# Kernel tuning notes

Measured on AMD Instinct MI355X. Metric: run time of the kernel, lower is better.

The kernel has to match this reference:

```python
import jax, jax.numpy as jnp
import numpy as np

# iRPE contextual+transposed, method=PRODUCT, rpe config ratio=1.9
ALPHA, BETA, GAMMA = 1.9, 3.8, 15.2
BETA_INT = int(BETA)            # 3
S = 2 * BETA_INT + 1            # 7
NUM_BUCKETS = S * S             # 49
B, H, D = 8, 8, 64
HEIGHT = WIDTH = 32
L = HEIGHT * WIDTH              # 1024, skip = L - height*width = 0


def _piecewise_index(rp):
    # numpy port of torch piecewise_index (no-grad, precomputed constant)
    rp = np.asarray(rp)
    rp_abs = np.abs(rp)
    safe = np.maximum(rp_abs.astype(np.float64), ALPHA)  # avoid log(0) under mask
    y = ALPHA + np.log(safe / ALPHA) / np.log(GAMMA / ALPHA) * (BETA - ALPHA)
    y = np.minimum(np.round(y), BETA)                    # round then clip(max=beta)
    out = np.where(rp_abs <= ALPHA, np.round(rp.astype(np.float64)), np.sign(rp) * y)
    return out.astype(np.int64)                          # trunc toward zero (+-3.8 -> +-3)


def _rp_bucket_product(height, width):
    pos = np.stack(np.meshgrid(np.arange(height), np.arange(width), indexing='ij'), -1)
    pos = pos.reshape(-1, 2)                             # (L, 2)
    diff = pos[:, None, :] - pos[None, :, :]             # (L, L, 2)
    r = _piecewise_index(diff[:, :, 0]) + BETA_INT
    c = _piecewise_index(diff[:, :, 1]) + BETA_INT
    return (r * S + c).astype(np.int32)                  # values in [0, 49)


def setup_inputs() -> dict:
    key = jax.random.key(0)
    k1, k2 = jax.random.split(key)
    x = jax.random.normal(k1, (B, H, L, D), dtype=jnp.float32)
    lookup_table_weight = jax.random.normal(k2, (H, D, NUM_BUCKETS), dtype=jnp.float32) * 0.02
    rp_bucket = jnp.asarray(_rp_bucket_product(HEIGHT, WIDTH))  # (L, L) int32 constant
    return {"x": x, "lookup_table_weight": lookup_table_weight, "rp_bucket": rp_bucket}


def reference(x, lookup_table_weight, rp_bucket):
    # x: (B, H, L, D); lookup_table_weight: (H, D, K); rp_bucket: (L, L) int
    # lt[b,h,l,k] = sum_d x[b,h,l,d] * W[h,d,k]
    lt = jnp.einsum('bhld,hdk->bhlk', x, lookup_table_weight)  # (B, H, L, K) small
    Lq = rp_bucket.shape[0]
    row = jnp.arange(Lq)[:, None]                              # (L, 1)
    # out[b,h,i,j] = lt[b,h,i,rp_bucket[i,j]] -- the big irregular gather
    return lt[:, :, row, rp_bucket]                            # (B, H, L, L)
```

## Files before the change

### kernel.cpp

```cpp
#include <hip/hip_runtime.h>


constexpr int cL = 1024;
constexpr int cD = 64;
constexpr int cK = 49;
constexpr int cBH = 64;
constexpr int cHALF = 32;

__global__ __launch_bounds__(256) void irpe_fused(
    const float* __restrict__ x,
    const float* __restrict__ W,
    const int*   __restrict__ bucket,
    float*       __restrict__ out)
{
    __shared__ float4 xs4[cHALF][cD / 4];
    __shared__ float  lts[cHALF * cK];

    const int gid  = blockIdx.x;
    const int i    = gid >> 1;
    const int bh0  = (gid & 1) * cHALF;
    const int tid  = threadIdx.x;

    const float4* x4 = (const float4*)x;
    #pragma unroll
    for (int r = 0; r < 2; ++r) {
        const int idx = r * 256 + tid;
        const int lh  = idx >> 4;
        const int d4  = idx & 15;
        xs4[lh][d4] = x4[((size_t)(bh0 + lh) * cL + i) * (cD / 4) + d4];
    }

    const int4 bk = ((const int4*)(bucket + (size_t)i * cL))[tid];

    __syncthreads();

    const float* xsf = (const float*)xs4;
    for (int p = tid; p < cHALF * cK; p += 256) {
        const int lh = p / cK;
        const int k  = p - lh * cK;
        const int h  = (bh0 + lh) & 7;
        const float* wp = W + (size_t)h * cD * cK + k;
        const float* xr = xsf + lh * cD;
        float acc = 0.0f;
        #pragma unroll
        for (int d = 0; d < cD; ++d) {
            acc = fmaf(xr[d], wp[(size_t)d * cK], acc);
        }
        lts[p] = acc;
    }
    __syncthreads();

    float4* obase = (float4*)(out + (size_t)bh0 * cL * cL + (size_t)i * cL);
    #pragma unroll 4
    for (int lh = 0; lh < cHALF; ++lh) {
        const float* lrow = lts + lh * cK;
        float4 o;
        o.x = lrow[bk.x];
        o.y = lrow[bk.y];
        o.z = lrow[bk.z];
        o.w = lrow[bk.w];
        obase[(size_t)lh * cL * (cL / 4) + tid] = o;
    }
}

extern "C" void kernel_launch(void* const* d_in, const int* in_sizes, int n_in,
                              void* d_out, int out_size, void* d_ws, size_t ws_size,
                              hipStream_t stream) {
    const float* x      = (const float*)d_in[0];
    const float* W      = (const float*)d_in[1];
    const int*   bucket = (const int*)d_in[2];
    float*       out    = (float*)d_out;

    const int grid = cL * 2;
    irpe_fused<<<grid, 256, 0, stream>>>(x, W, bucket, out);
}
```

Baseline: 320.4 us.

## Retile iRPE gather over 4 query rows by 16 batch-heads per block

Each block now covers 4 consecutive query rows and 16 batch-head slices instead of 1 row and 32 slices. Each wavefront owns 4 batch-heads and writes 4 contiguous output rows (16 KB) per slice. The bucket rows are held in 16 int4 registers per lane and reused across batch-heads. This is meant to give longer contiguous write streams and to amortize bucket loads, at the cost of more registers, more shared memory and a smaller grid of 1024 blocks.

```diff
diff --git a/kernel.cpp b/kernel.cpp
--- a/kernel.cpp
+++ b/kernel.cpp
@@ -4,62 +4,81 @@
 constexpr int cL = 1024;
 constexpr int cD = 64;
 constexpr int cK = 49;
-constexpr int cBH = 64;
-constexpr int cHALF = 32;
+constexpr int IG = 4;
+constexpr int BG = 16;
 
-__global__ __launch_bounds__(256) void irpe_fused(
+__global__ __launch_bounds__(256, 4) void irpe_fused(
     const float* __restrict__ x,
     const float* __restrict__ W,
     const int*   __restrict__ bucket,
     float*       __restrict__ out)
 {
-    __shared__ float4 xs4[cHALF][cD / 4];
-    __shared__ float  lts[cHALF * cK];
+    __shared__ float xs[BG * IG][cD];
+    __shared__ float lts[BG * IG * cK];
 
     const int gid  = blockIdx.x;
-    const int i    = gid >> 1;
-    const int bh0  = (gid & 1) * cHALF;
+    const int igrp = gid >> 2;
+    const int bhg  = gid & 3;
+    const int i0   = igrp * IG;
+    const int bh0  = bhg * BG;
     const int tid  = threadIdx.x;
+    const int lane = tid & 63;
+    const int w    = tid >> 6;
 
     const float4* x4 = (const float4*)x;
     #pragma unroll
-    for (int r = 0; r < 2; ++r) {
-        const int idx = r * 256 + tid;
-        const int lh  = idx >> 4;
+    for (int rr = 0; rr < 4; ++rr) {
+        const int idx = rr * 256 + tid;
+        const int row = idx >> 4;
         const int d4  = idx & 15;
-        xs4[lh][d4] = x4[((size_t)(bh0 + lh) * cL + i) * (cD / 4) + d4];
+        const int lhb = row >> 2;
+        const int li  = row & 3;
+        float4 v = x4[((size_t)(bh0 + lhb) * cL + (i0 + li)) * (cD / 4) + d4];
+        ((float4*)xs[row])[d4] = v;
     }
 
-    const int4 bk = ((const int4*)(bucket + (size_t)i * cL))[tid];
+    int4 bkt[IG * 4];
+    #pragma unroll
+    for (int t = 0; t < IG * 4; ++t) {
+        const int li = t >> 2;
+        const int jc = t & 3;
+        bkt[t] = ((const int4*)(bucket + (size_t)(i0 + li) * cL + jc * 256))[lane];
+    }
 
     __syncthreads();
 
-    const float* xsf = (const float*)xs4;
-    for (int p = tid; p < cHALF * cK; p += 256) {
-        const int lh = p / cK;
-        const int k  = p - lh * cK;
-        const int h  = (bh0 + lh) & 7;
+    for (int p = tid; p < BG * IG * cK; p += 256) {
+        const int row = p / cK;
+        const int k   = p - row * cK;
+        const int lhb = row >> 2;
+        const int h   = lhb & 7;
         const float* wp = W + (size_t)h * cD * cK + k;
-        const float* xr = xsf + lh * cD;
+        const float* xr = xs[row];
         float acc = 0.0f;
         #pragma unroll
-        for (int d = 0; d < cD; ++d) {
-            acc = fmaf(xr[d], wp[(size_t)d * cK], acc);
-        }
+        for (int d = 0; d < cD; ++d)
+            acc = fmaf(xr[d], wp[d * cK], acc);
         lts[p] = acc;
     }
     __syncthreads();
 
-    float4* obase = (float4*)(out + (size_t)bh0 * cL * cL + (size_t)i * cL);
-    #pragma unroll 4
-    for (int lh = 0; lh < cHALF; ++lh) {
-        const float* lrow = lts + lh * cK;
-        float4 o;
-        o.x = lrow[bk.x];
-        o.y = lrow[bk.y];
-        o.z = lrow[bk.z];
-        o.w = lrow[bk.w];
-        obase[(size_t)lh * cL * (cL / 4) + tid] = o;
+    #pragma unroll
+    for (int q = 0; q < 4; ++q) {
+        const int lhb = w * 4 + q;
+        float4* pb = (float4*)(out + ((size_t)(bh0 + lhb) * cL + i0) * cL);
+        const float* lbase = lts + lhb * (IG * cK);
+        #pragma unroll 4
+        for (int t = 0; t < IG * 4; ++t) {
+            const int li = t >> 2;
+            const float* lrow = lbase + li * cK;
+            const int4 bk = bkt[t];
+            float4 o;
+            o.x = lrow[bk.x];
+            o.y = lrow[bk.y];
+            o.z = lrow[bk.z];
+            o.w = lrow[bk.w];
+            pb[t * 64 + lane] = o;
+        }
     }
 }
 
@@ -71,6 +90,6 @@
     const int*   bucket = (const int*)d_in[2];
     float*       out    = (float*)d_out;
 
-    const int grid = cL * 2;
+    const int grid = (cL / IG) * (64 / BG);
     irpe_fused<<<grid, 256, 0, stream>>>(x, W, bucket, out);
 }
```

New measurement: 347.2 us. 8.4% more time.
